# Optimization experiments

Measured on AMD Instinct MI355X. Metric: run time of the kernel, lower is better.

Reference implementation:

```python
import jax, jax.numpy as jnp
import numpy as np

N_GRAPHS = 1000
P = 300                 # nodes per ring graph
N = N_GRAPHS * P        # 300000 nodes
IN_DIM = 2
HID = 128
OUT_DIM = 2


def _ring_edges():
    idx = jnp.arange(N)
    g = idx // P
    pos = idx % P
    nxt = g * P + (pos + 1) % P
    src = jnp.concatenate([idx, nxt])
    dst = jnp.concatenate([nxt, idx])
    return jnp.stack([src, dst]), g


def setup_inputs() -> dict:
    key = jax.random.key(0)
    ks = jax.random.split(key, 11)
    edge_index, batch = _ring_edges()
    x = jax.random.normal(ks[0], (N, IN_DIM), jnp.float32)

    def glorot(k, fan_in, fan_out):
        lim = np.sqrt(6.0 / (fan_in + fan_out)).astype(np.float32)
        return jax.random.uniform(k, (fan_in, fan_out), jnp.float32, -lim, lim)

    return {
        "x": x,
        "edge_index": edge_index,
        "batch": batch,
        "W1": glorot(ks[1], IN_DIM, HID), "b1": jnp.zeros((HID,), jnp.float32),
        "W2": glorot(ks[2], HID, HID),    "b2": jnp.zeros((HID,), jnp.float32),
        "W3": glorot(ks[3], HID, HID),    "b3": jnp.zeros((HID,), jnp.float32),
        "fw1": glorot(ks[4], HID, HID),   "fb1": jnp.zeros((HID,), jnp.float32),
        "fw2": glorot(ks[5], HID, OUT_DIM), "fb2": jnp.zeros((OUT_DIM,), jnp.float32),
    }


def _gcn_conv(x, W, b, src, dst, norm):
    h = x @ W                              # [N, out]
    msg = h[src] * norm[:, None]           # gather + per-edge scale
    agg = jax.ops.segment_sum(msg, dst, num_segments=N)  # scatter-add
    return agg + b


def reference(x, edge_index, batch, W1, b1, W2, b2, W3, b3, fw1, fb1, fw2, fb2):
    loop = jnp.arange(N)
    src = jnp.concatenate([edge_index[0], loop])
    dst = jnp.concatenate([edge_index[1], loop])
    deg = jax.ops.segment_sum(jnp.ones_like(dst, jnp.float32), dst, num_segments=N)
    dis = jax.lax.rsqrt(deg)               # deg >= 1 due to self-loops
    norm = dis[src] * dis[dst]             # per-edge normalization

    h = jax.nn.relu(_gcn_conv(x, W1, b1, src, dst, norm))
    h = jax.nn.relu(_gcn_conv(h, W2, b2, src, dst, norm))
    h = jax.nn.relu(_gcn_conv(h, W3, b3, src, dst, norm))

    # global mean pool per graph
    sums = jax.ops.segment_sum(h, batch, num_segments=N_GRAPHS)
    cnts = jax.ops.segment_sum(jnp.ones((N,), jnp.float32), batch, num_segments=N_GRAPHS)
    pooled = sums / cnts[:, None]

    out = jax.nn.relu(pooled @ fw1 + fb1)
    out = out @ fw2 + fb2
    return out
```

## Files before the change

kernel.cpp:

```cpp
#include <hip/hip_runtime.h>
#include <hip/hip_bf16.h>
#include <stdint.h>

#define P    300
#define HID  128
#define NG   1000
#define NTL  19

typedef __attribute__((ext_vector_type(8))) short bf16x8;
typedef __attribute__((ext_vector_type(4))) float f32x4;

__device__ short g_wsw[2 * HID * HID];

__device__ __forceinline__ short f2bf(float f) {
    union { float f; uint32_t u; } v; v.f = f;
    uint32_t r = v.u + 0x7fffu + ((v.u >> 16) & 1u);
    return (short)(r >> 16);
}
__device__ __forceinline__ float bf2f(short s) {
    union { uint32_t u; float f; } v; v.u = ((uint32_t)(uint16_t)s) << 16;
    return v.f;
}
__device__ __forceinline__ uint32_t pkbf2(float a, float b) {
    union { __hip_bfloat162 h; uint32_t u; } cv;
    cv.h = __float22bfloat162_rn(float2{a, b});
    return cv.u;
}
__device__ __forceinline__ float unpk(int v, int ft) {
    return bf2f((short)(ft ? (((uint32_t)v) >> 16) : (v & 0xffff)));
}

__global__ __launch_bounds__(256) void k_prep(const float* __restrict__ W2,
                                              const float* __restrict__ W3) {
    int b = blockIdx.x;
    const bool perm = (b < 8);
    const float* W = perm ? W2 : W3;
    short* dst = g_wsw + (perm ? 0 : HID * HID);
    int t    = (b & 7) * 256 + threadIdx.x;
    int fkey = t >> 4;
    int kc   = t & 15;
    int fsrc;
    if (perm) {
        int u = fkey >> 5, ft = (fkey >> 4) & 1, l = fkey & 15;
        fsrc = u * 32 + 2 * l + ft;
    } else fsrc = fkey;
    bf16x8 o;
    #pragma unroll
    for (int j = 0; j < 8; ++j)
        o[j] = f2bf(W[(kc * 8 + j) * HID + fsrc]);
    *(bf16x8*)&dst[(fkey * 16 + (kc ^ (fkey & 15))) * 8] = o;
}

__device__ __forceinline__ void avg_epi(const float* G, float vp0, float vn3,
                                        float b, float* o) {
    o[0] = (vp0  + G[0] + G[1]) * (1.0f / 3.0f) + b;
    o[1] = (G[0] + G[1] + G[2]) * (1.0f / 3.0f) + b;
    o[2] = (G[1] + G[2] + G[3]) * (1.0f / 3.0f) + b;
    o[3] = (G[2] + G[3] + vn3 ) * (1.0f / 3.0f) + b;
    #pragma unroll
    for (int i = 0; i < 4; ++i) o[i] = o[i] > 0.f ? o[i] : 0.f;
}

template<int POOL>
__device__ __forceinline__ void run_pass(short* __restrict__ buf,
                                         const short* __restrict__ wbase,
                                         const float* __restrict__ bias,
                                         float* __restrict__ pool, int tid) {
    const int lane = tid & 63, wv = tid >> 6, q = lane >> 4, lm = lane & 15;
    const int ftg0 = wv * 2;
    bf16x8 wf[2][4];
    #pragma unroll
    for (int ft = 0; ft < 2; ++ft) {
        int fkey = (ftg0 + ft) * 16 + lm;
        #pragma unroll
        for (int kk = 0; kk < 4; ++kk)
            wf[ft][kk] = *(const bf16x8*)&wbase[(fkey * 16 + ((4 * kk + q) ^ lm)) * 8];
    }
    float biaf[2];
    #pragma unroll
    for (int ft = 0; ft < 2; ++ft)
        biaf[ft] = POOL ? bias[(ftg0 + ft) * 16 + lm] : bias[wv * 32 + 2 * lm + ft];
    const int sA = (q == 0) ? (48 + lm) : (lane - 16);
    const int sB = (lane + 16) & 63;
    const int fpair = wv * 32 + 2 * lm;
    const int kcs = fpair >> 3, offs = fpair & 7;

    f32x4 Gp[2], Ga[2], Gb[2], Gfirst[2];
    float c15[2] = {0.f, 0.f}, r0G1[2] = {0.f, 0.f};
    float psum[2] = {0.f, 0.f};

    auto mfma_tile = [&](int t, f32x4* G) {
        const short* tb = buf + t * 2048;
        G[0] = f32x4{0.f, 0.f, 0.f, 0.f};
        G[1] = f32x4{0.f, 0.f, 0.f, 0.f};
        #pragma unroll
        for (int kk = 0; kk < 4; ++kk) {
            bf16x8 af = *(const bf16x8*)&tb[(lm * 16 + ((4 * kk + q) ^ lm)) * 8];
            G[0] = __builtin_amdgcn_mfma_f32_16x16x32_bf16(af, wf[0][kk], G[0], 0, 0, 0);
            G[1] = __builtin_amdgcn_mfma_f32_16x16x32_bf16(af, wf[1][kk], G[1], 0, 0, 0);
        }
    };
    auto epi = [&](const f32x4* E, const f32x4* N, int T, bool act) -> int {
        uint32_t uA = pkbf2(E[0][3], E[1][3]);
        uint32_t uB = pkbf2(E[0][0], E[1][0]);
        uint32_t uC = pkbf2(N[0][0], N[1][0]);
        int vA = __shfl((int)uA, sA, 64);
        int vB = __shfl((int)uB, sB, 64);
        int vC = __shfl((int)uC, lm, 64);
        float o[2][4];
        #pragma unroll
        for (int ft = 0; ft < 2; ++ft) {
            float bpA = unpk(vA, ft), bpB = unpk(vB, ft), bpC = unpk(vC, ft);
            float vp0 = (q == 0) ? c15[ft] : bpA;
            float vn3 = (q == 3) ? bpC : bpB;
            avg_epi((const float*)&E[ft], vp0, vn3, biaf[ft], o[ft]);
            c15[ft] = bpA;
            if (act && POOL) psum[ft] += o[ft][0] + o[ft][1] + o[ft][2] + o[ft][3];
        }
        if (act && !POOL) {
            #pragma unroll
            for (int i = 0; i < 4; ++i) {
                int node = T * 16 + q * 4 + i;
                *(uint32_t*)&buf[(node * 16 + (kcs ^ (node & 15))) * 8 + offs] =
                    pkbf2(o[0][i], o[1][i]);
            }
        }
        return vC;
    };

    mfma_tile(0, Gp);
    Gfirst[0] = Gp[0]; Gfirst[1] = Gp[1];

    for (int j = 1; j <= 9; ++j) {
        mfma_tile(2 * j - 1, Ga);
        mfma_tile(2 * j, Gb);
        if (!POOL) __syncthreads();
        int vC0 = epi(Gp, Ga, 2 * j - 2, j > 1);
        if (j == 1) { r0G1[0] = unpk(vC0, 0); r0G1[1] = unpk(vC0, 1); }
        epi(Ga, Gb, 2 * j - 1, true);
        Gp[0] = Gb[0]; Gp[1] = Gb[1];
    }

    float o18[2][4], o0[2][4];
    #pragma unroll
    for (int ft = 0; ft < 2; ++ft) {
        float bpA  = __shfl(Gp[ft][3], sA, 64);
        float bpB  = __shfl(Gp[ft][0], sB, 64);
        float g0r0 = __shfl(Gfirst[ft][0], lm, 64);
        float vp0  = (q == 0) ? c15[ft] : bpA;
        float vn3  = (q == 2) ? g0r0 : bpB;
        avg_epi((const float*)&Gp[ft], vp0, vn3, biaf[ft], o18[ft]);
        float bpW  = __shfl(Gp[ft][3], 32 + lm, 64);
        float bpA0 = __shfl(Gfirst[ft][3], sA, 64);
        float bpB0 = __shfl(Gfirst[ft][0], sB, 64);
        float vp00 = (q == 0) ? bpW : bpA0;
        float vn30 = (q == 3) ? r0G1[ft] : bpB0;
        avg_epi((const float*)&Gfirst[ft], vp00, vn30, biaf[ft], o0[ft]);
        if (POOL) {
            if (q < 3) psum[ft] += o18[ft][0] + o18[ft][1] + o18[ft][2] + o18[ft][3];
            psum[ft] += o0[ft][0] + o0[ft][1] + o0[ft][2] + o0[ft][3];
        }
    }
    if (!POOL) {
        #pragma unroll
        for (int i = 0; i < 4; ++i) {
            if (q < 3) {
                int node = 288 + q * 4 + i;
                *(uint32_t*)&buf[(node * 16 + (kcs ^ (node & 15))) * 8 + offs] =
                    pkbf2(o18[0][i], o18[1][i]);
            }
            int n0 = q * 4 + i;
            *(uint32_t*)&buf[(n0 * 16 + (kcs ^ (n0 & 15))) * 8 + offs] =
                pkbf2(o0[0][i], o0[1][i]);
        }
    }

    if (POOL) {
        #pragma unroll
        for (int ft = 0; ft < 2; ++ft) {
            psum[ft] += __shfl_xor(psum[ft], 16, 64);
            psum[ft] += __shfl_xor(psum[ft], 32, 64);
        }
        if (q == 0) {
            pool[ftg0 * 16 + lm]      = psum[0];
            pool[ftg0 * 16 + 16 + lm] = psum[1];
        }
    }
}

__global__ __launch_bounds__(256, 2) void k_graph(
        const float* __restrict__ x,
        const float* __restrict__ W1,  const float* __restrict__ b1,
        const float* __restrict__ b2v, const float* __restrict__ b3v,
        const float* __restrict__ fw1, const float* __restrict__ fb1,
        const float* __restrict__ fw2, const float* __restrict__ fb2,
        float* __restrict__ out) {
    __shared__ __align__(16) short buf[304 * HID];
    __shared__ __align__(16) float scr[640];
    float* xs    = scr;
    float* pool  = scr;
    float* parts = scr + 128;
    float* s1    = scr + 384;

    const int g = blockIdx.x, tid = threadIdx.x;

    if (tid < 150) *(float4*)&xs[tid * 4] = *(const float4*)&x[g * 600 + tid * 4];
    __syncthreads();

    {
        const int kc1 = tid & 15;
        const int n0  = tid >> 4;
        float w1x[8], w1y[8], b1v[8];
        #pragma unroll
        for (int j = 0; j < 8; ++j) {
            w1x[j] = W1[kc1 * 8 + j];
            w1y[j] = W1[HID + kc1 * 8 + j];
            b1v[j] = b1[kc1 * 8 + j];
        }
        #pragma unroll
        for (int it = 0; it < NTL; ++it) {
            int node = it * 16 + n0;
            uint32_t w[4] = {0u, 0u, 0u, 0u};
            if (node < P) {
                int prev = (node == 0)     ? P - 1 : node - 1;
                int next = (node == P - 1) ? 0     : node + 1;
                float2 xp = *(const float2*)&xs[2 * prev];
                float2 xc = *(const float2*)&xs[2 * node];
                float2 xn = *(const float2*)&xs[2 * next];
                float ax = (xp.x + xc.x + xn.x) * (1.f / 3.f);
                float ay = (xp.y + xc.y + xn.y) * (1.f / 3.f);
                #pragma unroll
                for (int jj = 0; jj < 4; ++jj) {
                    float va = ax * w1x[2*jj]   + ay * w1y[2*jj]   + b1v[2*jj];
                    float vb = ax * w1x[2*jj+1] + ay * w1y[2*jj+1] + b1v[2*jj+1];
                    va = va > 0.f ? va : 0.f;
                    vb = vb > 0.f ? vb : 0.f;
                    w[jj] = pkbf2(va, vb);
                }
            }
            *(uint4*)&buf[(node * 16 + (kc1 ^ (node & 15))) * 8] =
                uint4{w[0], w[1], w[2], w[3]};
        }
    }
    __syncthreads();

    run_pass<0>(buf, g_wsw,             b2v, pool, tid);
    __syncthreads();
    run_pass<1>(buf, g_wsw + HID * HID, b3v, pool, tid);
    __syncthreads();

    {
        int f = tid & 127, half = tid >> 7;
        float p = 0.f;
        const float* fw1c = fw1 + f;
        #pragma unroll 4
        for (int k = half * 64; k < half * 64 + 64; ++k)
            p += pool[k] * fw1c[k * 128];
        parts[half * 128 + f] = p;
    }
    __syncthreads();
    if (tid < 128) {
        float o1 = fb1[tid] + (parts[tid] + parts[128 + tid]) * (1.0f / 300.0f);
        s1[tid] = o1 > 0.f ? o1 : 0.f;
    }
    __syncthreads();
    if (tid < 128) {
        int o = tid >> 6, ln = tid & 63;
        float v = s1[ln] * fw2[ln * 2 + o] + s1[ln + 64] * fw2[(ln + 64) * 2 + o];
        #pragma unroll
        for (int off = 1; off <= 32; off <<= 1)
            v += __shfl_xor(v, off, 64);
        if (ln == 0) out[g * 2 + o] = v + fb2[o];
    }
}

extern "C" void kernel_launch(void* const* d_in, const int* in_sizes, int n_in,
                              void* d_out, int out_size, void* d_ws, size_t ws_size,
                              hipStream_t stream) {
    const float* x   = (const float*)d_in[0];
    const float* W1  = (const float*)d_in[3];
    const float* b1  = (const float*)d_in[4];
    const float* W2  = (const float*)d_in[5];
    const float* b2  = (const float*)d_in[6];
    const float* W3  = (const float*)d_in[7];
    const float* b3  = (const float*)d_in[8];
    const float* fw1 = (const float*)d_in[9];
    const float* fb1 = (const float*)d_in[10];
    const float* fw2 = (const float*)d_in[11];
    const float* fb2 = (const float*)d_in[12];
    float* out = (float*)d_out;

    k_prep <<<dim3(16), dim3(256), 0, stream>>>(W2, W3);
    k_graph<<<dim3(NG), dim3(256), 0, stream>>>(x, W1, b1, b2, b3,
                                                fw1, fb1, fw2, fb2, out);
}
```

Baseline: 126.5 us.

## Split each ring graph into four halo-overlapped arcs across blocks with atomic pooling

Each graph is now handled by four blocks, each covering a 75-node arc plus a halo of recomputed neighbours, so shared memory per block drops and occupancy rises. Per-arc partial pool sums go to a global buffer through atomicAdd; that buffer is zeroed in the prep kernel. The FC head moves into a separate kernel launch. The cost is redundant halo work on overlapping nodes, global atomics, and an extra launch.

```diff
diff --git a/kernel.cpp b/kernel.cpp
--- a/kernel.cpp
+++ b/kernel.cpp
@@ -5,12 +5,14 @@
 #define P    300
 #define HID  128
 #define NG   1000
-#define NTL  19
+#define ARC  75
+#define NTT  5
 
 typedef __attribute__((ext_vector_type(8))) short bf16x8;
 typedef __attribute__((ext_vector_type(4))) float f32x4;
 
 __device__ short g_wsw[2 * HID * HID];
+__device__ float g_pool[NG * HID];
 
 __device__ __forceinline__ short f2bf(float f) {
     union { float f; uint32_t u; } v; v.f = f;
@@ -33,6 +35,12 @@
 __global__ __launch_bounds__(256) void k_prep(const float* __restrict__ W2,
                                               const float* __restrict__ W3) {
     int b = blockIdx.x;
+    int tz = b * 256 + threadIdx.x;
+    #pragma unroll
+    for (int i = 0; i < 32; ++i) {
+        int idx = i * 4096 + tz;
+        if (idx < NG * HID) g_pool[idx] = 0.f;
+    }
     const bool perm = (b < 8);
     const float* W = perm ? W2 : W3;
     short* dst = g_wsw + (perm ? 0 : HID * HID);
@@ -65,7 +73,7 @@
 __device__ __forceinline__ void run_pass(short* __restrict__ buf,
                                          const short* __restrict__ wbase,
                                          const float* __restrict__ bias,
-                                         float* __restrict__ pool, int tid) {
+                                         int gidx, int tid) {
     const int lane = tid & 63, wv = tid >> 6, q = lane >> 4, lm = lane & 15;
     const int ftg0 = wv * 2;
     bf16x8 wf[2][4];
@@ -85,93 +93,56 @@
     const int fpair = wv * 32 + 2 * lm;
     const int kcs = fpair >> 3, offs = fpair & 7;
 
-    f32x4 Gp[2], Ga[2], Gb[2], Gfirst[2];
-    float c15[2] = {0.f, 0.f}, r0G1[2] = {0.f, 0.f};
-    float psum[2] = {0.f, 0.f};
-
-    auto mfma_tile = [&](int t, f32x4* G) {
+    f32x4 G[NTT][2];
+    #pragma unroll
+    for (int t = 0; t < NTT; ++t) {
+        G[t][0] = f32x4{0.f, 0.f, 0.f, 0.f};
+        G[t][1] = f32x4{0.f, 0.f, 0.f, 0.f};
         const short* tb = buf + t * 2048;
-        G[0] = f32x4{0.f, 0.f, 0.f, 0.f};
-        G[1] = f32x4{0.f, 0.f, 0.f, 0.f};
         #pragma unroll
         for (int kk = 0; kk < 4; ++kk) {
             bf16x8 af = *(const bf16x8*)&tb[(lm * 16 + ((4 * kk + q) ^ lm)) * 8];
-            G[0] = __builtin_amdgcn_mfma_f32_16x16x32_bf16(af, wf[0][kk], G[0], 0, 0, 0);
-            G[1] = __builtin_amdgcn_mfma_f32_16x16x32_bf16(af, wf[1][kk], G[1], 0, 0, 0);
-        }
-    };
-    auto epi = [&](const f32x4* E, const f32x4* N, int T, bool act) -> int {
-        uint32_t uA = pkbf2(E[0][3], E[1][3]);
-        uint32_t uB = pkbf2(E[0][0], E[1][0]);
-        uint32_t uC = pkbf2(N[0][0], N[1][0]);
+            G[t][0] = __builtin_amdgcn_mfma_f32_16x16x32_bf16(af, wf[0][kk], G[t][0], 0, 0, 0);
+            G[t][1] = __builtin_amdgcn_mfma_f32_16x16x32_bf16(af, wf[1][kk], G[t][1], 0, 0, 0);
+        }
+    }
+    if (!POOL) __syncthreads();
+
+    float c15[2] = {0.f, 0.f};
+    float psum[2] = {0.f, 0.f};
+    #pragma unroll
+    for (int t = 0; t < NTT; ++t) {
+        const int tn = (t < NTT - 1) ? t + 1 : t;
+        uint32_t uA = pkbf2(G[t][0][3],  G[t][1][3]);
+        uint32_t uB = pkbf2(G[t][0][0],  G[t][1][0]);
+        uint32_t uC = pkbf2(G[tn][0][0], G[tn][1][0]);
         int vA = __shfl((int)uA, sA, 64);
         int vB = __shfl((int)uB, sB, 64);
         int vC = __shfl((int)uC, lm, 64);
-        float o[2][4];
+        float o2[2][4];
         #pragma unroll
         for (int ft = 0; ft < 2; ++ft) {
             float bpA = unpk(vA, ft), bpB = unpk(vB, ft), bpC = unpk(vC, ft);
             float vp0 = (q == 0) ? c15[ft] : bpA;
             float vn3 = (q == 3) ? bpC : bpB;
-            avg_epi((const float*)&E[ft], vp0, vn3, biaf[ft], o[ft]);
+            avg_epi((const float*)&G[t][ft], vp0, vn3, biaf[ft], o2[ft]);
             c15[ft] = bpA;
-            if (act && POOL) psum[ft] += o[ft][0] + o[ft][1] + o[ft][2] + o[ft][3];
-        }
-        if (act && !POOL) {
+            if (POOL) {
+                #pragma unroll
+                for (int i = 0; i < 4; ++i) {
+                    int r = t * 16 + q * 4 + i;
+                    if (r >= 2 && r <= 76) psum[ft] += o2[ft][i];
+                }
+            }
+        }
+        if (!POOL) {
             #pragma unroll
             for (int i = 0; i < 4; ++i) {
-                int node = T * 16 + q * 4 + i;
-                *(uint32_t*)&buf[(node * 16 + (kcs ^ (node & 15))) * 8 + offs] =
-                    pkbf2(o[0][i], o[1][i]);
+                int r = t * 16 + q * 4 + i;
+                if (r >= 1 && r <= 77)
+                    *(uint32_t*)&buf[(r * 16 + (kcs ^ (r & 15))) * 8 + offs] =
+                        pkbf2(o2[0][i], o2[1][i]);
             }
-        }
-        return vC;
-    };
-
-    mfma_tile(0, Gp);
-    Gfirst[0] = Gp[0]; Gfirst[1] = Gp[1];
-
-    for (int j = 1; j <= 9; ++j) {
-        mfma_tile(2 * j - 1, Ga);
-        mfma_tile(2 * j, Gb);
-        if (!POOL) __syncthreads();
-        int vC0 = epi(Gp, Ga, 2 * j - 2, j > 1);
-        if (j == 1) { r0G1[0] = unpk(vC0, 0); r0G1[1] = unpk(vC0, 1); }
-        epi(Ga, Gb, 2 * j - 1, true);
-        Gp[0] = Gb[0]; Gp[1] = Gb[1];
-    }
-
-    float o18[2][4], o0[2][4];
-    #pragma unroll
-    for (int ft = 0; ft < 2; ++ft) {
-        float bpA  = __shfl(Gp[ft][3], sA, 64);
-        float bpB  = __shfl(Gp[ft][0], sB, 64);
-        float g0r0 = __shfl(Gfirst[ft][0], lm, 64);
-        float vp0  = (q == 0) ? c15[ft] : bpA;
-        float vn3  = (q == 2) ? g0r0 : bpB;
-        avg_epi((const float*)&Gp[ft], vp0, vn3, biaf[ft], o18[ft]);
-        float bpW  = __shfl(Gp[ft][3], 32 + lm, 64);
-        float bpA0 = __shfl(Gfirst[ft][3], sA, 64);
-        float bpB0 = __shfl(Gfirst[ft][0], sB, 64);
-        float vp00 = (q == 0) ? bpW : bpA0;
-        float vn30 = (q == 3) ? r0G1[ft] : bpB0;
-        avg_epi((const float*)&Gfirst[ft], vp00, vn30, biaf[ft], o0[ft]);
-        if (POOL) {
-            if (q < 3) psum[ft] += o18[ft][0] + o18[ft][1] + o18[ft][2] + o18[ft][3];
-            psum[ft] += o0[ft][0] + o0[ft][1] + o0[ft][2] + o0[ft][3];
-        }
-    }
-    if (!POOL) {
-        #pragma unroll
-        for (int i = 0; i < 4; ++i) {
-            if (q < 3) {
-                int node = 288 + q * 4 + i;
-                *(uint32_t*)&buf[(node * 16 + (kcs ^ (node & 15))) * 8 + offs] =
-                    pkbf2(o18[0][i], o18[1][i]);
-            }
-            int n0 = q * 4 + i;
-            *(uint32_t*)&buf[(n0 * 16 + (kcs ^ (n0 & 15))) * 8 + offs] =
-                pkbf2(o0[0][i], o0[1][i]);
         }
     }
 
@@ -182,29 +153,29 @@
             psum[ft] += __shfl_xor(psum[ft], 32, 64);
         }
         if (q == 0) {
-            pool[ftg0 * 16 + lm]      = psum[0];
-            pool[ftg0 * 16 + 16 + lm] = psum[1];
-        }
-    }
-}
-
-__global__ __launch_bounds__(256, 2) void k_graph(
+            atomicAdd(&g_pool[gidx * HID + ftg0 * 16 + lm],      psum[0]);
+            atomicAdd(&g_pool[gidx * HID + ftg0 * 16 + 16 + lm], psum[1]);
+        }
+    }
+}
+
+__global__ __launch_bounds__(256, 4) void k_graph(
         const float* __restrict__ x,
         const float* __restrict__ W1,  const float* __restrict__ b1,
-        const float* __restrict__ b2v, const float* __restrict__ b3v,
-        const float* __restrict__ fw1, const float* __restrict__ fb1,
-        const float* __restrict__ fw2, const float* __restrict__ fb2,
-        float* __restrict__ out) {
-    __shared__ __align__(16) short buf[304 * HID];
-    __shared__ __align__(16) float scr[640];
-    float* xs    = scr;
-    float* pool  = scr;
-    float* parts = scr + 128;
-    float* s1    = scr + 384;
-
-    const int g = blockIdx.x, tid = threadIdx.x;
-
-    if (tid < 150) *(float4*)&xs[tid * 4] = *(const float4*)&x[g * 600 + tid * 4];
+        const float* __restrict__ b2v, const float* __restrict__ b3v) {
+    __shared__ __align__(16) short buf[NTT * 16 * HID];
+    __shared__ __align__(16) float xs[164];
+
+    const int g   = blockIdx.x >> 2;
+    const int s   = (blockIdx.x & 3) * ARC;
+    const int tid = threadIdx.x;
+
+    if (tid < 81) {
+        int node = s - 3 + tid;
+        node += (node < 0) ? P : 0;
+        node -= (node >= P) ? P : 0;
+        *(float2*)&xs[2 * tid] = *(const float2*)&x[g * 600 + node * 2];
+    }
     __syncthreads();
 
     {
@@ -218,15 +189,13 @@
             b1v[j] = b1[kc1 * 8 + j];
         }
         #pragma unroll
-        for (int it = 0; it < NTL; ++it) {
-            int node = it * 16 + n0;
+        for (int it = 0; it < NTT; ++it) {
+            int r = it * 16 + n0;
             uint32_t w[4] = {0u, 0u, 0u, 0u};
-            if (node < P) {
-                int prev = (node == 0)     ? P - 1 : node - 1;
-                int next = (node == P - 1) ? 0     : node + 1;
-                float2 xp = *(const float2*)&xs[2 * prev];
-                float2 xc = *(const float2*)&xs[2 * node];
-                float2 xn = *(const float2*)&xs[2 * next];
+            if (r < 79) {
+                float2 xp = *(const float2*)&xs[2 * r];
+                float2 xc = *(const float2*)&xs[2 * r + 2];
+                float2 xn = *(const float2*)&xs[2 * r + 4];
                 float ax = (xp.x + xc.x + xn.x) * (1.f / 3.f);
                 float ay = (xp.y + xc.y + xn.y) * (1.f / 3.f);
                 #pragma unroll
@@ -238,34 +207,34 @@
                     w[jj] = pkbf2(va, vb);
                 }
             }
-            *(uint4*)&buf[(node * 16 + (kc1 ^ (node & 15))) * 8] =
+            *(uint4*)&buf[(r * 16 + (kc1 ^ (r & 15))) * 8] =
                 uint4{w[0], w[1], w[2], w[3]};
         }
     }
     __syncthreads();
 
-    run_pass<0>(buf, g_wsw,             b2v, pool, tid);
-    __syncthreads();
-    run_pass<1>(buf, g_wsw + HID * HID, b3v, pool, tid);
-    __syncthreads();
-
+    run_pass<0>(buf, g_wsw,             b2v, g, tid);
+    __syncthreads();
+    run_pass<1>(buf, g_wsw + HID * HID, b3v, g, tid);
+}
+
+__global__ __launch_bounds__(128) void k_fc(const float* __restrict__ fw1,
+                                            const float* __restrict__ fb1,
+                                            const float* __restrict__ fw2,
+                                            const float* __restrict__ fb2,
+                                            float* __restrict__ out) {
+    int g = blockIdx.x, f = threadIdx.x;
+    __shared__ float pl[128];
+    __shared__ float s1[128];
+    pl[f] = g_pool[g * HID + f] * (1.0f / 300.0f);
+    __syncthreads();
+    float o1 = fb1[f];
+    #pragma unroll 8
+    for (int k = 0; k < 128; ++k) o1 += pl[k] * fw1[k * 128 + f];
+    s1[f] = o1 > 0.f ? o1 : 0.f;
+    __syncthreads();
     {
-        int f = tid & 127, half = tid >> 7;
-        float p = 0.f;
-        const float* fw1c = fw1 + f;
-        #pragma unroll 4
-        for (int k = half * 64; k < half * 64 + 64; ++k)
-            p += pool[k] * fw1c[k * 128];
-        parts[half * 128 + f] = p;
-    }
-    __syncthreads();
-    if (tid < 128) {
-        float o1 = fb1[tid] + (parts[tid] + parts[128 + tid]) * (1.0f / 300.0f);
-        s1[tid] = o1 > 0.f ? o1 : 0.f;
-    }
-    __syncthreads();
-    if (tid < 128) {
-        int o = tid >> 6, ln = tid & 63;
+        int o = f >> 6, ln = f & 63;
         float v = s1[ln] * fw2[ln * 2 + o] + s1[ln + 64] * fw2[(ln + 64) * 2 + o];
         #pragma unroll
         for (int off = 1; off <= 32; off <<= 1)
@@ -290,7 +259,7 @@
     const float* fb2 = (const float*)d_in[12];
     float* out = (float*)d_out;
 
-    k_prep <<<dim3(16), dim3(256), 0, stream>>>(W2, W3);
-    k_graph<<<dim3(NG), dim3(256), 0, stream>>>(x, W1, b1, b2, b3,
-                                                fw1, fb1, fw2, fb2, out);
-}
+    k_prep <<<dim3(16),     dim3(256), 0, stream>>>(W2, W3);
+    k_graph<<<dim3(NG * 4), dim3(256), 0, stream>>>(x, W1, b1, b2, b3);
+    k_fc   <<<dim3(NG),     dim3(128), 0, stream>>>(fw1, fb1, fw2, fb2, out);
+}
```

New measurement: 131.6 us. 1.04x slower.
